# Kernel tuning notes

Measured on AMD Instinct MI355X. Metric: run time of the kernel, lower is better.

The kernel has to match this reference:

```python
import jax, jax.numpy as jnp
import numpy as np

N_NODES = 50000
N_EDGES = 800000
IN_F, E_F, OUT_F = 128, 32, 128

def setup_inputs() -> dict:
    key = jax.random.key(0)
    ks = jax.random.split(key, 8)
    return {
        "h": jax.random.normal(ks[0], (N_NODES, IN_F), dtype=jnp.float32),
        "eftr": jax.random.normal(ks[1], (N_EDGES, E_F), dtype=jnp.float32),
        "weight": jax.random.normal(ks[2], (IN_F + E_F, OUT_F), dtype=jnp.float32) * (1.0 / np.sqrt(IN_F + E_F)),
        "W_w": jax.random.normal(ks[3], (OUT_F, IN_F + OUT_F), dtype=jnp.float32) * (1.0 / np.sqrt(IN_F + OUT_F)),
        "W_b": jax.random.normal(ks[4], (OUT_F,), dtype=jnp.float32) * 0.01,
        "bias": jnp.zeros((OUT_F,), dtype=jnp.float32),
        "src_idx": jax.random.randint(ks[5], (N_EDGES,), 0, N_NODES, dtype=jnp.int64) if jax.config.jax_enable_x64 else jax.random.randint(ks[5], (N_EDGES,), 0, N_NODES, dtype=jnp.int32),
        "dst_idx": jax.random.randint(ks[6], (N_EDGES,), 0, N_NODES, dtype=jnp.int32),
        "num_dst": N_NODES,
    }

def reference(h, eftr, weight, W_w, W_b, bias, src_idx, dst_idx, num_dst):
    # Segment-mean of concat([h[src], eftr]) over dst neighborhoods.
    # Sum node part and edge part separately (avoids materializing the concat mailbox).
    sum_h = jax.ops.segment_sum(h[src_idx], dst_idx, num_segments=num_dst)   # [D, IN_F]
    sum_e = jax.ops.segment_sum(eftr, dst_idx, num_segments=num_dst)        # [D, E_F]
    cnt = jax.ops.segment_sum(jnp.ones((dst_idx.shape[0],), h.dtype), dst_idx, num_segments=num_dst)
    denom = jnp.maximum(cnt, 1.0)[:, None]  # zero-degree nodes -> h_neigh = 0
    feat_mean = jnp.concatenate([sum_h / denom, sum_e / denom], axis=-1)    # [D, IN_F+E_F]
    h_neigh = feat_mean @ weight                                            # [D, OUT_F]
    h_dst = h[:num_dst]
    h_prime = jnp.concatenate([h_dst, h_neigh], axis=1) @ W_w.T + W_b       # Linear W
    h_prime = h_prime + bias
    return h_prime
```

## Files before the change

kernel.cpp:

```cpp
#include <hip/hip_runtime.h>

#define NN   50000
#define NE   800000
#define INF  128
#define EF   32
#define OUTF 128
#define KDIM 288
#define NBLK ((NN + 1023) / 1024)

typedef __attribute__((ext_vector_type(8))) short     short8;
typedef __attribute__((ext_vector_type(8))) unsigned short ushort8;
typedef __attribute__((ext_vector_type(4))) float     float4v;

__device__ __forceinline__ unsigned short f2bf(float f) {
    union { float f; unsigned int u; } c; c.f = f;
    const unsigned int r = (c.u + 0x7FFFu + ((c.u >> 16) & 1u)) >> 16;
    return (unsigned short)r;
}

__global__ void prep_kernel(const float* __restrict__ weight,
                            const float* __restrict__ W_w,
                            const float* __restrict__ W_b,
                            const float* __restrict__ bias,
                            float* __restrict__ Mmat,
                            float* __restrict__ cvec) {
    __shared__ float wrow[OUTF];
    const int r = blockIdx.x;
    const int j = threadIdx.x;
    if (r < 128) {
        Mmat[r * OUTF + j] = W_w[j * 256 + r];
        return;
    }
    if (r == KDIM) {
        cvec[j] = W_b[j] + bias[j];
        return;
    }
    const int m = r - 128;
    wrow[j] = weight[m * OUTF + j];
    __syncthreads();
    float acc = 0.f;
#pragma unroll 8
    for (int k = 0; k < OUTF; ++k)
        acc += wrow[k] * W_w[j * 256 + 128 + k];
    Mmat[r * OUTF + j] = acc;
}

__global__ void pack_kernel(const float* __restrict__ Mmat,
                            unsigned short* __restrict__ Mb) {
    const int b = blockIdx.x;
    const int kb = b >> 3;
    const int ct = b & 7;
    const int lane = threadIdx.x;
    const int col = ct * 16 + (lane & 15);
    const int k0 = kb * 32 + (lane >> 4) * 8;
    ushort8 v;
#pragma unroll
    for (int i = 0; i < 8; ++i)
        v[i] = f2bf(Mmat[(size_t)(k0 + i) * OUTF + col]);
    *(ushort8*)(Mb + ((size_t)(b * 64 + lane) * 8)) = v;
}

__global__ __launch_bounds__(256)
void cvt_h_kernel(const float* __restrict__ h, unsigned short* __restrict__ hb) {
    const size_t i = (size_t)(blockIdx.x * 256 + threadIdx.x) * 8;
    const float4 a = *(const float4*)(h + i);
    const float4 b = *(const float4*)(h + i + 4);
    ushort8 v;
    v[0] = f2bf(a.x); v[1] = f2bf(a.y); v[2] = f2bf(a.z); v[3] = f2bf(a.w);
    v[4] = f2bf(b.x); v[5] = f2bf(b.y); v[6] = f2bf(b.z); v[7] = f2bf(b.w);
    *(ushort8*)(hb + i) = v;
}

__global__ __launch_bounds__(256)
void hist_kernel(const int* __restrict__ dst, int* __restrict__ off) {
    const int e = (blockIdx.x * 256 + threadIdx.x) * 4;
    if (e < NE) {
        const int4 d = *(const int4*)(dst + e);
        atomicAdd(&off[d.x], 1);
        atomicAdd(&off[d.y], 1);
        atomicAdd(&off[d.z], 1);
        atomicAdd(&off[d.w], 1);
    }
}

__global__ __launch_bounds__(256)
void scan1_kernel(const int* __restrict__ off, int* __restrict__ partial) {
    const int b = blockIdx.x;
    const int tid = threadIdx.x;
    const int idx = b * 1024 + tid * 4;
    int v0 = 0, v1 = 0, v2 = 0, v3 = 0;
    if (idx + 3 < NN) {
        const int4 q = *(const int4*)(off + idx);
        v0 = q.x; v1 = q.y; v2 = q.z; v3 = q.w;
    } else {
        if (idx + 0 < NN) v0 = off[idx + 0];
        if (idx + 1 < NN) v1 = off[idx + 1];
        if (idx + 2 < NN) v2 = off[idx + 2];
    }
    int t = v0 + v1 + v2 + v3;
#pragma unroll
    for (int ofs = 32; ofs > 0; ofs >>= 1) t += __shfl_down(t, ofs);
    __shared__ int wsum[4];
    if ((tid & 63) == 0) wsum[tid >> 6] = t;
    __syncthreads();
    if (tid == 0) partial[b] = wsum[0] + wsum[1] + wsum[2] + wsum[3];
}

__global__ __launch_bounds__(256)
void scan3_kernel(int* __restrict__ off, const int* __restrict__ partial) {
    __shared__ int blockbase;
    __shared__ int wsum[4];
    const int b = blockIdx.x;
    const int tid = threadIdx.x;
    const int lane = tid & 63;
    const int wid = tid >> 6;

    if (wid == 0) {
        const int v = (lane < NBLK) ? partial[lane] : 0;
        int x = v;
#pragma unroll
        for (int ofs = 1; ofs < 64; ofs <<= 1) {
            const int t = __shfl_up(x, ofs);
            if (lane >= ofs) x += t;
        }
        if (lane == b) blockbase = x - v;
    }

    const int idx = b * 1024 + tid * 4;
    int v0 = 0, v1 = 0, v2 = 0, v3 = 0;
    if (idx + 3 < NN) {
        const int4 q = *(const int4*)(off + idx);
        v0 = q.x; v1 = q.y; v2 = q.z; v3 = q.w;
    } else {
        if (idx + 0 < NN) v0 = off[idx + 0];
        if (idx + 1 < NN) v1 = off[idx + 1];
        if (idx + 2 < NN) v2 = off[idx + 2];
    }
    const int tsum = v0 + v1 + v2 + v3;
    int x = tsum;
#pragma unroll
    for (int ofs = 1; ofs < 64; ofs <<= 1) {
        const int t = __shfl_up(x, ofs);
        if (lane >= ofs) x += t;
    }
    if (lane == 63) wsum[wid] = x;
    __syncthreads();
    int wp = 0;
    for (int w = 0; w < wid; ++w) wp += wsum[w];
    const int base = blockbase + wp + (x - tsum);
    if (idx + 0 < NN) off[idx + 0] = base;
    if (idx + 1 < NN) off[idx + 1] = base + v0;
    if (idx + 2 < NN) off[idx + 2] = base + v0 + v1;
    if (idx + 3 < NN) off[idx + 3] = base + v0 + v1 + v2;
}

__global__ __launch_bounds__(256)
void scatter_ids_kernel(const int* __restrict__ srcv,
                        const int* __restrict__ dst,
                        int* __restrict__ off,
                        int2* __restrict__ eo2) {
    const int e = (blockIdx.x * 256 + threadIdx.x) * 4;
    if (e < NE) {
        const int4 s = *(const int4*)(srcv + e);
        const int4 d = *(const int4*)(dst + e);
        int p;
        p = atomicAdd(&off[d.x], 1); eo2[p] = make_int2(s.x, e + 0);
        p = atomicAdd(&off[d.y], 1); eo2[p] = make_int2(s.y, e + 1);
        p = atomicAdd(&off[d.z], 1); eo2[p] = make_int2(s.z, e + 2);
        p = atomicAdd(&off[d.w], 1); eo2[p] = make_int2(s.w, e + 3);
    }
}

__global__ __launch_bounds__(256)
void gather_kernel(const unsigned short* __restrict__ hb,
                   const float* __restrict__ eftr,
                   const int* __restrict__ off,
                   const int2* __restrict__ eo2,
                   unsigned short* __restrict__ mean_h,
                   unsigned short* __restrict__ mean_e) {
    const int tid = threadIdx.x;
    const int lane = tid & 63;
    const int node = blockIdx.x * 4 + (tid >> 6);
    if (node >= NN) return;

    const int end = off[node];
    const int start = (node == 0) ? 0 : off[node - 1];

    float ax = 0.f, ay = 0.f, ae = 0.f;
    const unsigned short* hcol = hb + lane * 2;
    const int el = lane & 31;
    const bool lowhalf = (lane < 32);

    for (int base = start; base < end; base += 64) {
        const int m = min(64, end - base);
        int px = 0, py = 0;
        if (base + lane < end) {
            const long long pv =
                __builtin_nontemporal_load((const long long*)(eo2 + base + lane));
            px = (int)pv;
            py = (int)(pv >> 32);
        }
        int j = 0;
        for (; j + 7 < m; j += 8) {
            int s[8], e[8];
#pragma unroll
            for (int u = 0; u < 8; ++u) {
                s[u] = __builtin_amdgcn_readlane(px, j + u);
                e[u] = __builtin_amdgcn_readlane(py, j + u);
            }
            unsigned v[8];
#pragma unroll
            for (int u = 0; u < 8; ++u)
                v[u] = *(const unsigned*)(hcol + (size_t)s[u] * INF);
            float f[4];
#pragma unroll
            for (int u = 0; u < 4; ++u) {
                const int ee = lowhalf ? e[2 * u] : e[2 * u + 1];
                f[u] = __builtin_nontemporal_load(&eftr[(size_t)ee * EF + el]);
            }
#pragma unroll
            for (int u = 0; u < 8; ++u) {
                union { unsigned u; float f; } lo, hi;
                lo.u = v[u] << 16;
                hi.u = v[u] & 0xffff0000u;
                ax += lo.f; ay += hi.f;
            }
            ae += (f[0] + f[1]) + (f[2] + f[3]);
        }
        for (; j < m; ++j) {
            const int s0 = __builtin_amdgcn_readlane(px, j);
            const int e0 = __builtin_amdgcn_readlane(py, j);
            const unsigned v0 = *(const unsigned*)(hcol + (size_t)s0 * INF);
            union { unsigned u; float f; } lo, hi;
            lo.u = v0 << 16;
            hi.u = v0 & 0xffff0000u;
            ax += lo.f; ay += hi.f;
            if (lowhalf) ae += __builtin_nontemporal_load(&eftr[(size_t)e0 * EF + el]);
        }
    }

    ae += __shfl(ae, lane + 32);

    const float inv = 1.f / fmaxf((float)(end - start), 1.f);
    const unsigned mx = f2bf(ax * inv);
    const unsigned my = f2bf(ay * inv);
    *(unsigned*)(mean_h + (size_t)node * INF + lane * 2) = mx | (my << 16);
    if (lowhalf) mean_e[(size_t)node * EF + el] = f2bf(ae * inv);
}

__global__ __launch_bounds__(256)
void node_gemm_kernel(const unsigned short* __restrict__ hb,
                      const unsigned short* __restrict__ mean_h,
                      const unsigned short* __restrict__ mean_e,
                      const unsigned short* __restrict__ Mb,
                      const float* __restrict__ cvec,
                      float* __restrict__ out) {
    const int tid = threadIdx.x;
    const int lane = tid & 63;
    const int wid = tid >> 6;
    const int nt = blockIdx.x * 4 + wid;
    const int m16 = lane & 15;
    const int quad = lane >> 4;
    const int koff = quad * 8;

    const int anode = nt * 16 + m16;
    const int nclamp = (anode < NN) ? anode : (NN - 1);

    float4v acc[8] = {};

    for (int kb = 0; kb < 9; ++kb) {
        const unsigned short* srcp;
        if (kb < 4)
            srcp = hb + (size_t)nclamp * INF + kb * 32 + koff;
        else if (kb < 8)
            srcp = mean_h + (size_t)nclamp * INF + (kb - 4) * 32 + koff;
        else
            srcp = mean_e + (size_t)nclamp * EF + koff;
        const short8 a = *(const short8*)(const void*)srcp;

        const short8* bp = (const short8*)(Mb + (size_t)kb * 8 * 64 * 8);
#pragma unroll
        for (int ct = 0; ct < 8; ++ct) {
            const short8 b = bp[ct * 64 + lane];
            acc[ct] = __builtin_amdgcn_mfma_f32_16x16x32_bf16(a, b, acc[ct], 0, 0, 0);
        }
    }

    float cv[8];
#pragma unroll
    for (int ct = 0; ct < 8; ++ct) cv[ct] = cvec[ct * 16 + m16];

#pragma unroll
    for (int r = 0; r < 4; ++r) {
        const int nrow = nt * 16 + quad * 4 + r;
        if (nrow < NN) {
            float* orow = out + (size_t)nrow * OUTF;
#pragma unroll
            for (int ct = 0; ct < 8; ++ct)
                orow[ct * 16 + m16] = acc[ct][r] + cv[ct];
        }
    }
}

extern "C" void kernel_launch(void* const* d_in, const int* in_sizes, int n_in,
                              void* d_out, int out_size, void* d_ws, size_t ws_size,
                              hipStream_t stream) {
    const float* h      = (const float*)d_in[0];
    const float* eftr   = (const float*)d_in[1];
    const float* weight = (const float*)d_in[2];
    const float* W_w    = (const float*)d_in[3];
    const float* W_b    = (const float*)d_in[4];
    const float* bias   = (const float*)d_in[5];
    const int*   src    = (const int*)d_in[6];
    const int*   dst    = (const int*)d_in[7];
    float* out = (float*)d_out;

    char* base = (char*)d_ws;
    unsigned short* mean_h = (unsigned short*)(base);
    unsigned short* mean_e = (unsigned short*)(base + 12800000);
    unsigned short* h_bf   = (unsigned short*)(base + 16000000);
    float* Mmat            = (float*)(base + 28800000);
    float* cvec            = (float*)(base + 28947456);
    unsigned short* Mb     = (unsigned short*)(base + 28947968);
    int*   off             = (int*)(base + 29021696);
    int2*  eo2             = (int2*)(base + 29221696);
    int*   partial         = (int*)(base + 35621696);

    hipMemsetAsync(off, 0, (size_t)NN * sizeof(int), stream);

    prep_kernel<<<KDIM + 1, 128, 0, stream>>>(weight, W_w, W_b, bias, Mmat, cvec);
    pack_kernel<<<72, 64, 0, stream>>>(Mmat, Mb);
    cvt_h_kernel<<<3125, 256, 0, stream>>>(h, h_bf);
    hist_kernel<<<(NE / 4 + 255) / 256, 256, 0, stream>>>(dst, off);
    scan1_kernel<<<NBLK, 256, 0, stream>>>(off, partial);
    scan3_kernel<<<NBLK, 256, 0, stream>>>(off, partial);
    scatter_ids_kernel<<<(NE / 4 + 255) / 256, 256, 0, stream>>>(src, dst, off, eo2);
    gather_kernel<<<(NN + 3) / 4, 256, 0, stream>>>(h_bf, eftr, off, eo2,
                                                    mean_h, mean_e);
    node_gemm_kernel<<<(NN / 64) + 1, 256, 0, stream>>>(h_bf, mean_h, mean_e,
                                                        Mb, cvec, out);
}
```

Baseline: 325.6 us.

## Gather four edges per wave with wide row loads; fuse cvt and histogram

The gather kernel now splits each wave into four 16-lane groups. Each group handles a different edge and loads a 16-byte slice of the bf16 row, with ds_bpermute replacing scalar readlane broadcasts. Partial sums are reduced with cross-group shuffles at the end, and a zero pad row lets invalid lanes load safely without branching. The h conversion and dst histogram are merged into one launch, and output stores become nontemporal. Wider per-lane loads and more edges in flight per wave are meant to raise memory-level parallelism in the random gather, at the cost of extra shuffle reductions and padded work on tail edges.

```diff
diff --git a/kernel.cpp b/kernel.cpp
--- a/kernel.cpp
+++ b/kernel.cpp
@@ -7,10 +7,12 @@
 #define OUTF 128
 #define KDIM 288
 #define NBLK ((NN + 1023) / 1024)
+#define CVT_BLKS 3125
 
 typedef __attribute__((ext_vector_type(8))) short     short8;
 typedef __attribute__((ext_vector_type(8))) unsigned short ushort8;
 typedef __attribute__((ext_vector_type(4))) float     float4v;
+typedef __attribute__((ext_vector_type(2))) float     float2v;
 
 __device__ __forceinline__ unsigned short f2bf(float f) {
     union { float f; unsigned int u; } c; c.f = f;
@@ -61,19 +63,29 @@
 }
 
 __global__ __launch_bounds__(256)
-void cvt_h_kernel(const float* __restrict__ h, unsigned short* __restrict__ hb) {
-    const size_t i = (size_t)(blockIdx.x * 256 + threadIdx.x) * 8;
-    const float4 a = *(const float4*)(h + i);
-    const float4 b = *(const float4*)(h + i + 4);
-    ushort8 v;
-    v[0] = f2bf(a.x); v[1] = f2bf(a.y); v[2] = f2bf(a.z); v[3] = f2bf(a.w);
-    v[4] = f2bf(b.x); v[5] = f2bf(b.y); v[6] = f2bf(b.z); v[7] = f2bf(b.w);
-    *(ushort8*)(hb + i) = v;
-}
-
-__global__ __launch_bounds__(256)
-void hist_kernel(const int* __restrict__ dst, int* __restrict__ off) {
-    const int e = (blockIdx.x * 256 + threadIdx.x) * 4;
+void cvt_hist_kernel(const float* __restrict__ h,
+                     unsigned short* __restrict__ hb,
+                     const int* __restrict__ dst,
+                     int* __restrict__ off) {
+    const int b = blockIdx.x;
+    if (b < CVT_BLKS) {
+        const size_t i = (size_t)(b * 256 + threadIdx.x) * 8;
+        const float4 a0 = *(const float4*)(h + i);
+        const float4 a1 = *(const float4*)(h + i + 4);
+        ushort8 v;
+        v[0] = f2bf(a0.x); v[1] = f2bf(a0.y); v[2] = f2bf(a0.z); v[3] = f2bf(a0.w);
+        v[4] = f2bf(a1.x); v[5] = f2bf(a1.y); v[6] = f2bf(a1.z); v[7] = f2bf(a1.w);
+        *(ushort8*)(hb + i) = v;
+        return;
+    }
+    if (b == CVT_BLKS) {
+        if (threadIdx.x < 16) {
+            ushort8 z = {};
+            *(ushort8*)(hb + (size_t)NN * INF + threadIdx.x * 8) = z;
+        }
+        return;
+    }
+    const int e = ((b - CVT_BLKS - 1) * 256 + threadIdx.x) * 4;
     if (e < NE) {
         const int4 d = *(const int4*)(dst + e);
         atomicAdd(&off[d.x], 1);
@@ -186,66 +198,69 @@
     const int end = off[node];
     const int start = (node == 0) ? 0 : off[node - 1];
 
-    float ax = 0.f, ay = 0.f, ae = 0.f;
-    const unsigned short* hcol = hb + lane * 2;
-    const int el = lane & 31;
-    const bool lowhalf = (lane < 32);
+    const int ql = lane & 15;
+    const int qg = lane >> 4;
+
+    float ax[8] = {0.f, 0.f, 0.f, 0.f, 0.f, 0.f, 0.f, 0.f};
+    float aex = 0.f, aey = 0.f;
 
     for (int base = start; base < end; base += 64) {
         const int m = min(64, end - base);
         int px = 0, py = 0;
-        if (base + lane < end) {
+        if (lane < m) {
             const long long pv =
                 __builtin_nontemporal_load((const long long*)(eo2 + base + lane));
             px = (int)pv;
             py = (int)(pv >> 32);
         }
-        int j = 0;
-        for (; j + 7 < m; j += 8) {
-            int s[8], e[8];
-#pragma unroll
-            for (int u = 0; u < 8; ++u) {
-                s[u] = __builtin_amdgcn_readlane(px, j + u);
-                e[u] = __builtin_amdgcn_readlane(py, j + u);
+        for (int j = 0; j < m; j += 8) {
+#pragma unroll
+            for (int u = 0; u < 2; ++u) {
+                const int eidx = j + u * 4 + qg;
+                const bool valid = eidx < m;
+                const int bidx = (eidx & 63) * 4;
+                int s = __builtin_amdgcn_ds_bpermute(bidx, px);
+                int e = __builtin_amdgcn_ds_bpermute(bidx, py);
+                s = valid ? s : NN;
+                e = valid ? e : 0;
+
+                const uint4 hv = *(const uint4*)(hb + (size_t)s * INF + ql * 8);
+#pragma unroll
+                for (int k = 0; k < 4; ++k) {
+                    const unsigned w = (&hv.x)[k];
+                    union { unsigned u; float f; } lo, hi;
+                    lo.u = w << 16;
+                    hi.u = w & 0xffff0000u;
+                    ax[2 * k]     += lo.f;
+                    ax[2 * k + 1] += hi.f;
+                }
+
+                const float2v ev = __builtin_nontemporal_load(
+                    (const float2v*)(eftr + (size_t)e * EF + ql * 2));
+                aex += valid ? ev.x : 0.f;
+                aey += valid ? ev.y : 0.f;
             }
-            unsigned v[8];
-#pragma unroll
-            for (int u = 0; u < 8; ++u)
-                v[u] = *(const unsigned*)(hcol + (size_t)s[u] * INF);
-            float f[4];
-#pragma unroll
-            for (int u = 0; u < 4; ++u) {
-                const int ee = lowhalf ? e[2 * u] : e[2 * u + 1];
-                f[u] = __builtin_nontemporal_load(&eftr[(size_t)ee * EF + el]);
-            }
-#pragma unroll
-            for (int u = 0; u < 8; ++u) {
-                union { unsigned u; float f; } lo, hi;
-                lo.u = v[u] << 16;
-                hi.u = v[u] & 0xffff0000u;
-                ax += lo.f; ay += hi.f;
-            }
-            ae += (f[0] + f[1]) + (f[2] + f[3]);
-        }
-        for (; j < m; ++j) {
-            const int s0 = __builtin_amdgcn_readlane(px, j);
-            const int e0 = __builtin_amdgcn_readlane(py, j);
-            const unsigned v0 = *(const unsigned*)(hcol + (size_t)s0 * INF);
-            union { unsigned u; float f; } lo, hi;
-            lo.u = v0 << 16;
-            hi.u = v0 & 0xffff0000u;
-            ax += lo.f; ay += hi.f;
-            if (lowhalf) ae += __builtin_nontemporal_load(&eftr[(size_t)e0 * EF + el]);
-        }
-    }
-
-    ae += __shfl(ae, lane + 32);
-
-    const float inv = 1.f / fmaxf((float)(end - start), 1.f);
-    const unsigned mx = f2bf(ax * inv);
-    const unsigned my = f2bf(ay * inv);
-    *(unsigned*)(mean_h + (size_t)node * INF + lane * 2) = mx | (my << 16);
-    if (lowhalf) mean_e[(size_t)node * EF + el] = f2bf(ae * inv);
+        }
+    }
+
+#pragma unroll
+    for (int k = 0; k < 8; ++k) {
+        ax[k] += __shfl_xor(ax[k], 16);
+        ax[k] += __shfl_xor(ax[k], 32);
+    }
+    aex += __shfl_xor(aex, 16); aex += __shfl_xor(aex, 32);
+    aey += __shfl_xor(aey, 16); aey += __shfl_xor(aey, 32);
+
+    if (qg == 0) {
+        const float inv = 1.f / fmaxf((float)(end - start), 1.f);
+        ushort8 mv;
+#pragma unroll
+        for (int k = 0; k < 8; ++k) mv[k] = f2bf(ax[k] * inv);
+        *(ushort8*)(mean_h + (size_t)node * INF + ql * 8) = mv;
+        const unsigned me =
+            (unsigned)f2bf(aex * inv) | ((unsigned)f2bf(aey * inv) << 16);
+        *(unsigned*)(mean_e + (size_t)node * EF + ql * 2) = me;
+    }
 }
 
 __global__ __launch_bounds__(256)
@@ -297,7 +312,8 @@
             float* orow = out + (size_t)nrow * OUTF;
 #pragma unroll
             for (int ct = 0; ct < 8; ++ct)
-                orow[ct * 16 + m16] = acc[ct][r] + cv[ct];
+                __builtin_nontemporal_store(acc[ct][r] + cv[ct],
+                                            &orow[ct * 16 + m16]);
         }
     }
 }
@@ -319,19 +335,19 @@
     unsigned short* mean_h = (unsigned short*)(base);
     unsigned short* mean_e = (unsigned short*)(base + 12800000);
     unsigned short* h_bf   = (unsigned short*)(base + 16000000);
-    float* Mmat            = (float*)(base + 28800000);
-    float* cvec            = (float*)(base + 28947456);
-    unsigned short* Mb     = (unsigned short*)(base + 28947968);
-    int*   off             = (int*)(base + 29021696);
-    int2*  eo2             = (int2*)(base + 29221696);
-    int*   partial         = (int*)(base + 35621696);
+    float* Mmat            = (float*)(base + 28800512);
+    float* cvec            = (float*)(base + 28947968);
+    unsigned short* Mb     = (unsigned short*)(base + 28948480);
+    int*   off             = (int*)(base + 29022208);
+    int2*  eo2             = (int2*)(base + 29222208);
+    int*   partial         = (int*)(base + 35622208);
 
     hipMemsetAsync(off, 0, (size_t)NN * sizeof(int), stream);
 
     prep_kernel<<<KDIM + 1, 128, 0, stream>>>(weight, W_w, W_b, bias, Mmat, cvec);
     pack_kernel<<<72, 64, 0, stream>>>(Mmat, Mb);
-    cvt_h_kernel<<<3125, 256, 0, stream>>>(h, h_bf);
-    hist_kernel<<<(NE / 4 + 255) / 256, 256, 0, stream>>>(dst, off);
+    cvt_hist_kernel<<<CVT_BLKS + 1 + (NE / 4 + 255) / 256, 256, 0, stream>>>(
+        h, h_bf, dst, off);
     scan1_kernel<<<NBLK, 256, 0, stream>>>(off, partial);
     scan3_kernel<<<NBLK, 256, 0, stream>>>(off, partial);
     scatter_ids_kernel<<<(NE / 4 + 255) / 256, 256, 0, stream>>>(src, dst, off, eo2);
```

Result: no change. 324.1 us (-0.5%).
